# Kernel tuning notes

Hardware: AMD Instinct MI355X
Metric: run time of the kernel (lower is better)

## Reference

```python
import jax, jax.numpy as jnp
import numpy as np

B, S, D = 4, 2048, 512
H, DK, DV = 8, 64, 64
EPS = 1e-6
MASK_FILL = -1e-9  # faithful to the original masked_fill value (NOT -inf)


def setup_inputs() -> dict:
    key = jax.random.key(0)
    ks = jax.random.split(key, 9)
    sc = 0.05
    return {
        "q": jax.random.normal(ks[0], (B, S, D), jnp.float32),
        "k": jax.random.normal(ks[1], (B, S, D), jnp.float32),
        "v": jax.random.normal(ks[2], (B, S, D), jnp.float32),
        "src_mask": jax.random.randint(ks[3], (B, S), 0, 2, jnp.int32),
        "Wq": jax.random.normal(ks[4], (D, H * DK), jnp.float32) * sc,
        "Wk": jax.random.normal(ks[5], (D, H * DK), jnp.float32) * sc,
        "Wv": jax.random.normal(ks[6], (D, H * DV), jnp.float32) * sc,
        "Wo": jax.random.normal(ks[7], (H * DV, D), jnp.float32) * sc,
        "gamma": jnp.ones((D,), jnp.float32),
        "beta": jnp.zeros((D,), jnp.float32),
    }


def reference(q, k, v, src_mask, Wq, Wk, Wv, Wo, gamma, beta):
    b, len_q, _ = q.shape
    residual = q
    # QKV projections -> [B, H, S, dk/dv]
    qh = (q @ Wq).reshape(b, len_q, H, DK).transpose(0, 2, 1, 3)
    kh = (k @ Wk).reshape(b, -1, H, DK).transpose(0, 2, 1, 3)
    vh = (v @ Wv).reshape(b, -1, H, DV).transpose(0, 2, 1, 3)
    # scores [B, H, S, S]
    attn = jnp.einsum('bhqd,bhkd->bhqk', qh, kh) / jnp.sqrt(jnp.float32(DK))
    # pairwise src mask: outer product of [B,S] mask, diagonal forced to 1
    sm = src_mask[:, :len_q].astype(jnp.float32)
    am = sm[:, :, None] * sm[:, None, :]               # [B, S, S]
    idx = jnp.arange(len_q)
    am = am.at[:, idx, idx].set(1.0)
    attn = jnp.where(am[:, None, :, :] == 0, MASK_FILL, attn)
    attn = jax.nn.softmax(attn, axis=-1)
    out = jnp.einsum('bhqk,bhkd->bhqd', attn, vh)      # [B, H, S, dv]
    out = out.transpose(0, 2, 1, 3).reshape(b, len_q, H * DV)
    out = out @ Wo + residual
    # LayerNorm(eps=1e-6)
    mu = jnp.mean(out, axis=-1, keepdims=True)
    var = jnp.var(out, axis=-1, keepdims=True)
    out = (out - mu) * jax.lax.rsqrt(var + EPS) * gamma + beta
    return out, attn
```

## Files before the change

kernel.cpp:

```cpp
#include <hip/hip_runtime.h>
#include <math.h>

#define B_ 4
#define S_ 2048
#define D_ 512
#define H_ 8
#define NEG_FILL (-1e-9f)

typedef __attribute__((ext_vector_type(8))) short bf16x8;
typedef __attribute__((ext_vector_type(4))) float f32x4;

#define MFMA16(A, Bm, C) __builtin_amdgcn_mfma_f32_16x16x32_bf16((A), (Bm), (C), 0, 0, 0)

__device__ __forceinline__ short f2b(float f) {
  union { float f; unsigned u; } x;
  x.f = f;
  unsigned r = x.u + 0x7fffu + ((x.u >> 16) & 1u);
  return (short)(r >> 16);
}

__global__ __launch_bounds__(256) void prep_wt(
    const float* __restrict__ Wq, const float* __restrict__ Wk,
    const float* __restrict__ Wv, const float* __restrict__ Wo,
    short* __restrict__ Wqt, short* __restrict__ Wkt,
    short* __restrict__ Wvt, short* __restrict__ Wot)
{
  const float* W; short* Wt;
  switch (blockIdx.z) {
    case 0: W = Wq; Wt = Wqt; break;
    case 1: W = Wk; Wt = Wkt; break;
    case 2: W = Wv; Wt = Wvt; break;
    default: W = Wo; Wt = Wot; break;
  }
  __shared__ float Ws[64 * 68];
  const int t = threadIdx.x;
  const int n0 = blockIdx.x * 64, k0 = blockIdx.y * 64;

  #pragma unroll
  for (int rep = 0; rep < 4; ++rep) {
    int e4 = rep * 256 + t;
    int r = e4 >> 4, c0 = (e4 & 15) * 4;
    *(float4*)&Ws[r * 68 + c0] = *(const float4*)&W[(size_t)(k0 + r) * 512 + n0 + c0];
  }
  __syncthreads();

  int rn = t >> 2;
  int kb = (t & 3) * 16;
  union { short s[8]; int4 v; } pk;
  #pragma unroll
  for (int half = 0; half < 2; ++half) {
    #pragma unroll
    for (int i = 0; i < 8; ++i)
      pk.s[i] = f2b(Ws[(kb + half * 8 + i) * 68 + rn]);
    *(int4*)&Wt[(size_t)(n0 + rn) * 512 + k0 + kb + half * 8] = pk.v;
  }
}

__global__ __launch_bounds__(256) void qkv_mfma(
    const float* __restrict__ q, const float* __restrict__ k, const float* __restrict__ v,
    const short* __restrict__ Wqt, const short* __restrict__ Wkt, const short* __restrict__ Wvt,
    short* __restrict__ qh, short* __restrict__ kh, short* __restrict__ vt)
{
  const int z = blockIdx.z;
  const float* X = (z == 0) ? q : (z == 1) ? k : v;
  const short* Wt = (z == 0) ? Wqt : (z == 1) ? Wkt : Wvt;

  __shared__ short Xs[64 * 72];
  __shared__ short Wsh[64 * 72];

  const int t = threadIdx.x;
  const int wave = t >> 6, lane = t & 63, quad = lane >> 4, l15 = lane & 15;
  const int tile_n = blockIdx.x * 64;
  const int tile_m = blockIdx.y * 64;

  f32x4 acc[4];
  #pragma unroll
  for (int nt = 0; nt < 4; ++nt) acc[nt] = (f32x4){0.f, 0.f, 0.f, 0.f};

  for (int k0 = 0; k0 < 512; k0 += 64) {
    __syncthreads();
    #pragma unroll
    for (int rep = 0; rep < 4; ++rep) {
      int e4 = rep * 256 + t;
      int row = e4 >> 4, c0 = (e4 & 15) * 4;
      float4 xv = *(const float4*)&X[(size_t)(tile_m + row) * 512 + k0 + c0];
      *(short4*)&Xs[row * 72 + c0] =
          make_short4(f2b(xv.x), f2b(xv.y), f2b(xv.z), f2b(xv.w));
    }
    #pragma unroll
    for (int rep = 0; rep < 2; ++rep) {
      int e = rep * 256 + t;
      int row = e >> 3, c0 = (e & 7) * 8;
      *(int4*)&Wsh[row * 72 + c0] = *(const int4*)&Wt[(size_t)(tile_n + row) * 512 + k0 + c0];
    }
    __syncthreads();
    #pragma unroll
    for (int ks = 0; ks < 2; ++ks) {
      bf16x8 af = *(bf16x8*)&Xs[(wave * 16 + l15) * 72 + ks * 32 + quad * 8];
      #pragma unroll
      for (int nt = 0; nt < 4; ++nt) {
        bf16x8 bfr = *(bf16x8*)&Wsh[(nt * 16 + l15) * 72 + ks * 32 + quad * 8];
        acc[nt] = MFMA16(af, bfr, acc[nt]);
      }
    }
  }

  const int h = tile_n >> 6;
  if (z < 2) {
    short* Y = (z == 0) ? qh : kh;
    #pragma unroll
    for (int nt = 0; nt < 4; ++nt) {
      int d = nt * 16 + l15;
      #pragma unroll
      for (int r = 0; r < 4; ++r) {
        int row = tile_m + wave * 16 + quad * 4 + r;
        int b = row >> 11, s = row & (S_ - 1);
        Y[(((size_t)(b * H_ + h)) * S_ + s) * 64 + d] = f2b(acc[nt][r]);
      }
    }
  } else {
    int row0 = tile_m + wave * 16 + quad * 4;
    int b = row0 >> 11, s0 = row0 & (S_ - 1);
    #pragma unroll
    for (int nt = 0; nt < 4; ++nt) {
      int d = nt * 16 + l15;
      short4 pk = make_short4(f2b(acc[nt][0]), f2b(acc[nt][1]),
                              f2b(acc[nt][2]), f2b(acc[nt][3]));
      *(short4*)&vt[(((size_t)(b * H_ + h)) * 64 + d) * S_ + s0] = pk;
    }
  }
}

__global__ __launch_bounds__(256) void attn_mfma(
    const short* __restrict__ qh, const short* __restrict__ kh,
    const short* __restrict__ vt, const int* __restrict__ src_mask,
    float* __restrict__ attn_out, short* __restrict__ ohb)
{
  const int t = threadIdx.x;
  const int wave = t >> 6, lane = t & 63, quad = lane >> 4, l15 = lane & 15;

  const int lin = blockIdx.y * 32 + blockIdx.x;
  const int nl  = (lin & 7) * 128 + (lin >> 3);
  const int bh = nl >> 5, b = bh >> 3, h = bh & 7;
  const int q0 = (nl & 31) * 64;

  __shared__ __align__(16) short KV[4][64 * 64];
  __shared__ __align__(16) short Ps[4][16 * 72];
  __shared__ __align__(16) int smAll[S_];

  const short* __restrict__ khb = kh + (size_t)bh * S_ * 64;
  const short* __restrict__ vtb = vt + (size_t)bh * 64 * S_;

  const int sr = t >> 3, sc = t & 7;
  const int wofs0 = sr * 128 + ((sc ^ (sr & 7)) << 4);
  const int wofs1 = (sr + 32) * 128 + ((sc ^ (sr & 7)) << 4);
  const int rofs0 = ((quad ^ (l15 & 7)) << 4);
  const int rofs1 = (((4 + quad) ^ (l15 & 7)) << 4);

  const size_t qrow = (size_t)bh * S_ + q0 + wave * 16 + l15;
  const bf16x8 qf0 = *(const bf16x8*)&qh[qrow * 64 + quad * 8];
  const bf16x8 qf1 = *(const bf16x8*)&qh[qrow * 64 + 32 + quad * 8];

  int4 kreg0, kreg1, vreg0, vreg1;
  int4 mreg0 = *(const int4*)&src_mask[b * S_ + t * 4];
  int4 mreg1 = *(const int4*)&src_mask[b * S_ + (256 + t) * 4];
  kreg0 = *(const int4*)&khb[(size_t)sr * 64 + sc * 8];
  kreg1 = *(const int4*)&khb[(size_t)(sr + 32) * 64 + sc * 8];
  *(int4*)&smAll[t * 4] = mreg0;
  *(int4*)&smAll[(256 + t) * 4] = mreg1;
  *(int4*)((char*)KV[0] + wofs0) = kreg0;
  *(int4*)((char*)KV[0] + wofs1) = kreg1;
  __syncthreads();

  int rloc[4], mqr[4], qir[4];
  #pragma unroll
  for (int r = 0; r < 4; ++r) {
    rloc[r] = wave * 16 + quad * 4 + r;
    qir[r] = q0 + rloc[r];
    mqr[r] = smAll[qir[r]];
  }

  float rs[4] = {0.f, 0.f, 0.f, 0.f};
  for (int step = 0; step < 32; ++step) {
    const int kt0 = step * 64;
    const int cur = step & 1;
    if (step < 31) {
      kreg0 = *(const int4*)&khb[(size_t)(kt0 + 64 + sr) * 64 + sc * 8];
      kreg1 = *(const int4*)&khb[(size_t)(kt0 + 64 + sr + 32) * 64 + sc * 8];
    }
    const char* Kc = (const char*)KV[cur];
    #pragma unroll
    for (int nt = 0; nt < 4; ++nt) {
      bf16x8 kf0 = *(const bf16x8*)(Kc + (nt * 16 + l15) * 128 + rofs0);
      bf16x8 kf1 = *(const bf16x8*)(Kc + (nt * 16 + l15) * 128 + rofs1);
      f32x4 c = (f32x4){0.f, 0.f, 0.f, 0.f};
      c = MFMA16(qf0, kf0, c);
      c = MFMA16(qf1, kf1, c);
      int kj = kt0 + nt * 16 + l15;
      int mk = smAll[kj];
      #pragma unroll
      for (int r = 0; r < 4; ++r) {
        float ss = c[r] * 0.125f;
        bool keep = (mqr[r] & mk) || (qir[r] == kj);
        ss = keep ? ss : NEG_FILL;
        rs[r] += __expf(ss);
      }
    }
    if (step < 31) {
      *(int4*)((char*)KV[cur ^ 1] + wofs0) = kreg0;
      *(int4*)((char*)KV[cur ^ 1] + wofs1) = kreg1;
    }
    __syncthreads();
  }
  #pragma unroll
  for (int r = 0; r < 4; ++r) {
    float vsum = rs[r];
    vsum += __shfl_xor(vsum, 1);
    vsum += __shfl_xor(vsum, 2);
    vsum += __shfl_xor(vsum, 4);
    vsum += __shfl_xor(vsum, 8);
    rs[r] = 1.f / vsum;
  }

  f32x4 oacc[4];
  #pragma unroll
  for (int dt = 0; dt < 4; ++dt) oacc[dt] = (f32x4){0.f, 0.f, 0.f, 0.f};

  float* __restrict__ arow[4];
  #pragma unroll
  for (int r = 0; r < 4; ++r)
    arow[r] = attn_out + ((size_t)bh * S_ + q0 + rloc[r]) * S_;

  short* __restrict__ ps = Ps[wave];

  kreg0 = *(const int4*)&khb[(size_t)sr * 64 + sc * 8];
  kreg1 = *(const int4*)&khb[(size_t)(sr + 32) * 64 + sc * 8];
  vreg0 = *(const int4*)&vtb[(size_t)sr * S_ + sc * 8];
  vreg1 = *(const int4*)&vtb[(size_t)(sr + 32) * S_ + sc * 8];
  *(int4*)((char*)KV[0] + wofs0) = kreg0;
  *(int4*)((char*)KV[0] + wofs1) = kreg1;
  *(int4*)((char*)KV[2] + wofs0) = vreg0;
  *(int4*)((char*)KV[2] + wofs1) = vreg1;
  __syncthreads();

  for (int step = 0; step < 32; ++step) {
    const int kt0 = step * 64;
    const int cur = step & 1;
    if (step < 31) {
      kreg0 = *(const int4*)&khb[(size_t)(kt0 + 64 + sr) * 64 + sc * 8];
      kreg1 = *(const int4*)&khb[(size_t)(kt0 + 64 + sr + 32) * 64 + sc * 8];
      vreg0 = *(const int4*)&vtb[(size_t)sr * S_ + kt0 + 64 + sc * 8];
      vreg1 = *(const int4*)&vtb[(size_t)(sr + 32) * S_ + kt0 + 64 + sc * 8];
    }
    const char* Kc = (const char*)KV[cur];
    const char* Vc = (const char*)KV[2 + cur];
    #pragma unroll
    for (int nt = 0; nt < 4; ++nt) {
      bf16x8 kf0 = *(const bf16x8*)(Kc + (nt * 16 + l15) * 128 + rofs0);
      bf16x8 kf1 = *(const bf16x8*)(Kc + (nt * 16 + l15) * 128 + rofs1);
      f32x4 c = (f32x4){0.f, 0.f, 0.f, 0.f};
      c = MFMA16(qf0, kf0, c);
      c = MFMA16(qf1, kf1, c);
      int kj = kt0 + nt * 16 + l15;
      int mk = smAll[kj];
      #pragma unroll
      for (int r = 0; r < 4; ++r) {
        float ss = c[r] * 0.125f;
        bool keep = (mqr[r] & mk) || (qir[r] == kj);
        ss = keep ? ss : NEG_FILL;
        float p = __expf(ss) * rs[r];
        __builtin_nontemporal_store(p, &arow[r][kj]);
        ps[(quad * 4 + r) * 72 + nt * 16 + l15] = f2b(p);
      }
    }
    bf16x8 pf0 = *(bf16x8*)&ps[l15 * 72 + quad * 8];
    bf16x8 pf1 = *(bf16x8*)&ps[l15 * 72 + 32 + quad * 8];
    #pragma unroll
    for (int dt = 0; dt < 4; ++dt) {
      bf16x8 vf0 = *(const bf16x8*)(Vc + (dt * 16 + l15) * 128 + rofs0);
      bf16x8 vf1 = *(const bf16x8*)(Vc + (dt * 16 + l15) * 128 + rofs1);
      oacc[dt] = MFMA16(pf0, vf0, oacc[dt]);
      oacc[dt] = MFMA16(pf1, vf1, oacc[dt]);
    }
    if (step < 31) {
      *(int4*)((char*)KV[cur ^ 1] + wofs0) = kreg0;
      *(int4*)((char*)KV[cur ^ 1] + wofs1) = kreg1;
      *(int4*)((char*)KV[2 + (cur ^ 1)] + wofs0) = vreg0;
      *(int4*)((char*)KV[2 + (cur ^ 1)] + wofs1) = vreg1;
    }
    __syncthreads();
  }

  #pragma unroll
  for (int dt = 0; dt < 4; ++dt) {
    int d = h * 64 + dt * 16 + l15;
    #pragma unroll
    for (int r = 0; r < 4; ++r)
      ohb[((size_t)b * S_ + q0 + rloc[r]) * 512 + d] = f2b(oacc[dt][r]);
  }
}

__global__ __launch_bounds__(256) void out_mfma(
    const short* __restrict__ ohb, const short* __restrict__ Wot,
    const float* __restrict__ resid, float* __restrict__ out)
{
  __shared__ short Xs[64 * 72];
  __shared__ short Wsh[64 * 72];

  const int t = threadIdx.x;
  const int wave = t >> 6, lane = t & 63, quad = lane >> 4, l15 = lane & 15;
  const int tile_n = blockIdx.x * 64;
  const int tile_m = blockIdx.y * 64;

  f32x4 acc[4];
  #pragma unroll
  for (int nt = 0; nt < 4; ++nt) acc[nt] = (f32x4){0.f, 0.f, 0.f, 0.f};

  for (int k0 = 0; k0 < 512; k0 += 64) {
    __syncthreads();
    #pragma unroll
    for (int rep = 0; rep < 2; ++rep) {
      int e = rep * 256 + t;
      int row = e >> 3, c0 = (e & 7) * 8;
      *(int4*)&Xs[row * 72 + c0] = *(const int4*)&ohb[(size_t)(tile_m + row) * 512 + k0 + c0];
      *(int4*)&Wsh[row * 72 + c0] = *(const int4*)&Wot[(size_t)(tile_n + row) * 512 + k0 + c0];
    }
    __syncthreads();
    #pragma unroll
    for (int ks = 0; ks < 2; ++ks) {
      bf16x8 af = *(bf16x8*)&Xs[(wave * 16 + l15) * 72 + ks * 32 + quad * 8];
      #pragma unroll
      for (int nt = 0; nt < 4; ++nt) {
        bf16x8 bfr = *(bf16x8*)&Wsh[(nt * 16 + l15) * 72 + ks * 32 + quad * 8];
        acc[nt] = MFMA16(af, bfr, acc[nt]);
      }
    }
  }

  #pragma unroll
  for (int nt = 0; nt < 4; ++nt) {
    int c = tile_n + nt * 16 + l15;
    #pragma unroll
    for (int r = 0; r < 4; ++r) {
      size_t row = tile_m + wave * 16 + quad * 4 + r;
      out[row * 512 + c] = acc[nt][r] + resid[row * 512 + c];
    }
  }
}

__global__ __launch_bounds__(256) void ln_kernel(
    float* __restrict__ io, const float* __restrict__ gamma, const float* __restrict__ beta)
{
  const int wid  = threadIdx.x >> 6;
  const int lane = threadIdx.x & 63;
  const size_t row = (size_t)blockIdx.x * 4 + wid;
  const size_t base = row * 512 + lane * 8;

  float4 x0 = *(const float4*)&io[base];
  float4 x1 = *(const float4*)&io[base + 4];
  float xs[8] = {x0.x, x0.y, x0.z, x0.w, x1.x, x1.y, x1.z, x1.w};

  float s = 0.f, s2 = 0.f;
  #pragma unroll
  for (int i = 0; i < 8; ++i) { s += xs[i]; s2 = fmaf(xs[i], xs[i], s2); }
  #pragma unroll
  for (int m = 1; m < 64; m <<= 1) {
    s  += __shfl_xor(s, m);
    s2 += __shfl_xor(s2, m);
  }
  float mu  = s * (1.f / 512.f);
  float var = s2 * (1.f / 512.f) - mu * mu;
  float rsq = rsqrtf(var + 1e-6f);

  float4 g0 = *(const float4*)&gamma[lane * 8];
  float4 g1 = *(const float4*)&gamma[lane * 8 + 4];
  float4 b0 = *(const float4*)&beta[lane * 8];
  float4 b1 = *(const float4*)&beta[lane * 8 + 4];
  float gs[8] = {g0.x, g0.y, g0.z, g0.w, g1.x, g1.y, g1.z, g1.w};
  float bs[8] = {b0.x, b0.y, b0.z, b0.w, b1.x, b1.y, b1.z, b1.w};

  float ys[8];
  #pragma unroll
  for (int i = 0; i < 8; ++i) ys[i] = (xs[i] - mu) * rsq * gs[i] + bs[i];
  *(float4*)&io[base]     = make_float4(ys[0], ys[1], ys[2], ys[3]);
  *(float4*)&io[base + 4] = make_float4(ys[4], ys[5], ys[6], ys[7]);
}

extern "C" void kernel_launch(void* const* d_in, const int* in_sizes, int n_in,
                              void* d_out, int out_size, void* d_ws, size_t ws_size,
                              hipStream_t stream)
{
  const float* q     = (const float*)d_in[0];
  const float* k     = (const float*)d_in[1];
  const float* v     = (const float*)d_in[2];
  const int*  smask  = (const int*)d_in[3];
  const float* Wq    = (const float*)d_in[4];
  const float* Wk    = (const float*)d_in[5];
  const float* Wv    = (const float*)d_in[6];
  const float* Wo    = (const float*)d_in[7];
  const float* gamma = (const float*)d_in[8];
  const float* beta  = (const float*)d_in[9];

  float* out  = (float*)d_out;
  float* attn = out + (size_t)B_ * S_ * D_;

  short* wsS = (short*)d_ws;
  short* qh  = wsS;
  short* kh  = qh + 4194304;
  short* vt  = kh + 4194304;
  short* ohb = vt + 4194304;
  short* Wqt = ohb + 4194304;
  short* Wkt = Wqt + 262144;
  short* Wvt = Wkt + 262144;
  short* Wot = Wvt + 262144;

  prep_wt<<<dim3(8, 8, 4), 256, 0, stream>>>(Wq, Wk, Wv, Wo, Wqt, Wkt, Wvt, Wot);
  qkv_mfma<<<dim3(8, 128, 3), 256, 0, stream>>>(q, k, v, Wqt, Wkt, Wvt, qh, kh, vt);
  attn_mfma<<<dim3(32, 32), 256, 0, stream>>>(qh, kh, vt, smask, attn, ohb);
  out_mfma<<<dim3(8, 128), 256, 0, stream>>>(ohb, Wot, q, out);
  ln_kernel<<<2048, 256, 0, stream>>>(out, gamma, beta);
}
```

Measured before the change: 724.5 us.

## Enlarge QKV GEMM tiles to 128x128 and attention blocks to 128 queries

The QKV projection kernel moves from 64x64 to 128x128 output tiles, with each of its four waves computing a 64x64 sub-tile from a 4x4 set of MFMA accumulators, so each loaded X and W fragment is reused more. The attention kernel now runs 512 threads (8 waves) per block covering 128 query rows, so every K/V tile staged in shared memory serves twice as many queries and global K/V traffic per query is halved. In exchange, registers per thread rise in the GEMM, shared memory per block grows, and both kernels launch fewer blocks, which may lower occupancy.

```diff
diff --git a/kernel.cpp b/kernel.cpp
--- a/kernel.cpp
+++ b/kernel.cpp
@@ -65,22 +65,25 @@
   const float* X = (z == 0) ? q : (z == 1) ? k : v;
   const short* Wt = (z == 0) ? Wqt : (z == 1) ? Wkt : Wvt;
 
-  __shared__ short Xs[64 * 72];
-  __shared__ short Wsh[64 * 72];
+  __shared__ short Xs[128 * 72];
+  __shared__ short Wsh[128 * 72];
 
   const int t = threadIdx.x;
   const int wave = t >> 6, lane = t & 63, quad = lane >> 4, l15 = lane & 15;
-  const int tile_n = blockIdx.x * 64;
-  const int tile_m = blockIdx.y * 64;
-
-  f32x4 acc[4];
-  #pragma unroll
-  for (int nt = 0; nt < 4; ++nt) acc[nt] = (f32x4){0.f, 0.f, 0.f, 0.f};
+  const int wm = wave >> 1, wn = wave & 1;
+  const int tile_n = blockIdx.x * 128;
+  const int tile_m = blockIdx.y * 128;
+
+  f32x4 acc[4][4];
+  #pragma unroll
+  for (int mt = 0; mt < 4; ++mt)
+    #pragma unroll
+    for (int nt = 0; nt < 4; ++nt) acc[mt][nt] = (f32x4){0.f, 0.f, 0.f, 0.f};
 
   for (int k0 = 0; k0 < 512; k0 += 64) {
     __syncthreads();
     #pragma unroll
-    for (int rep = 0; rep < 4; ++rep) {
+    for (int rep = 0; rep < 8; ++rep) {
       int e4 = rep * 256 + t;
       int row = e4 >> 4, c0 = (e4 & 15) * 4;
       float4 xv = *(const float4*)&X[(size_t)(tile_m + row) * 512 + k0 + c0];
@@ -88,7 +91,7 @@
           make_short4(f2b(xv.x), f2b(xv.y), f2b(xv.z), f2b(xv.w));
     }
     #pragma unroll
-    for (int rep = 0; rep < 2; ++rep) {
+    for (int rep = 0; rep < 4; ++rep) {
       int e = rep * 256 + t;
       int row = e >> 3, c0 = (e & 7) * 8;
       *(int4*)&Wsh[row * 72 + c0] = *(const int4*)&Wt[(size_t)(tile_n + row) * 512 + k0 + c0];
@@ -96,42 +99,56 @@
     __syncthreads();
     #pragma unroll
     for (int ks = 0; ks < 2; ++ks) {
-      bf16x8 af = *(bf16x8*)&Xs[(wave * 16 + l15) * 72 + ks * 32 + quad * 8];
-      #pragma unroll
-      for (int nt = 0; nt < 4; ++nt) {
-        bf16x8 bfr = *(bf16x8*)&Wsh[(nt * 16 + l15) * 72 + ks * 32 + quad * 8];
-        acc[nt] = MFMA16(af, bfr, acc[nt]);
-      }
-    }
-  }
-
-  const int h = tile_n >> 6;
+      bf16x8 af[4], bfr[4];
+      #pragma unroll
+      for (int mt = 0; mt < 4; ++mt)
+        af[mt] = *(bf16x8*)&Xs[(wm * 64 + mt * 16 + l15) * 72 + ks * 32 + quad * 8];
+      #pragma unroll
+      for (int nt = 0; nt < 4; ++nt)
+        bfr[nt] = *(bf16x8*)&Wsh[(wn * 64 + nt * 16 + l15) * 72 + ks * 32 + quad * 8];
+      #pragma unroll
+      for (int mt = 0; mt < 4; ++mt)
+        #pragma unroll
+        for (int nt = 0; nt < 4; ++nt)
+          acc[mt][nt] = MFMA16(af[mt], bfr[nt], acc[mt][nt]);
+    }
+  }
+
+  const int col0 = tile_n + wn * 64;
   if (z < 2) {
     short* Y = (z == 0) ? qh : kh;
     #pragma unroll
     for (int nt = 0; nt < 4; ++nt) {
-      int d = nt * 16 + l15;
-      #pragma unroll
-      for (int r = 0; r < 4; ++r) {
-        int row = tile_m + wave * 16 + quad * 4 + r;
-        int b = row >> 11, s = row & (S_ - 1);
-        Y[(((size_t)(b * H_ + h)) * S_ + s) * 64 + d] = f2b(acc[nt][r]);
+      int cc = col0 + nt * 16 + l15;
+      int h = cc >> 6, d = cc & 63;
+      #pragma unroll
+      for (int mt = 0; mt < 4; ++mt) {
+        #pragma unroll
+        for (int r = 0; r < 4; ++r) {
+          int row = tile_m + wm * 64 + mt * 16 + quad * 4 + r;
+          int b = row >> 11, s = row & (S_ - 1);
+          Y[(((size_t)(b * H_ + h)) * S_ + s) * 64 + d] = f2b(acc[mt][nt][r]);
+        }
       }
     }
   } else {
-    int row0 = tile_m + wave * 16 + quad * 4;
-    int b = row0 >> 11, s0 = row0 & (S_ - 1);
     #pragma unroll
     for (int nt = 0; nt < 4; ++nt) {
-      int d = nt * 16 + l15;
-      short4 pk = make_short4(f2b(acc[nt][0]), f2b(acc[nt][1]),
-                              f2b(acc[nt][2]), f2b(acc[nt][3]));
-      *(short4*)&vt[(((size_t)(b * H_ + h)) * 64 + d) * S_ + s0] = pk;
-    }
-  }
-}
-
-__global__ __launch_bounds__(256) void attn_mfma(
+      int cc = col0 + nt * 16 + l15;
+      int h = cc >> 6, d = cc & 63;
+      #pragma unroll
+      for (int mt = 0; mt < 4; ++mt) {
+        int row0 = tile_m + wm * 64 + mt * 16 + quad * 4;
+        int b = row0 >> 11, s0 = row0 & (S_ - 1);
+        short4 pk = make_short4(f2b(acc[mt][nt][0]), f2b(acc[mt][nt][1]),
+                                f2b(acc[mt][nt][2]), f2b(acc[mt][nt][3]));
+        *(short4*)&vt[(((size_t)(b * H_ + h)) * 64 + d) * S_ + s0] = pk;
+      }
+    }
+  }
+}
+
+__global__ __launch_bounds__(512) void attn_mfma(
     const short* __restrict__ qh, const short* __restrict__ kh,
     const short* __restrict__ vt, const int* __restrict__ src_mask,
     float* __restrict__ attn_out, short* __restrict__ ohb)
@@ -139,21 +156,20 @@
   const int t = threadIdx.x;
   const int wave = t >> 6, lane = t & 63, quad = lane >> 4, l15 = lane & 15;
 
-  const int lin = blockIdx.y * 32 + blockIdx.x;
-  const int nl  = (lin & 7) * 128 + (lin >> 3);
-  const int bh = nl >> 5, b = bh >> 3, h = bh & 7;
-  const int q0 = (nl & 31) * 64;
+  const int lin = blockIdx.y * 16 + blockIdx.x;
+  const int nl  = (lin & 7) * 64 + (lin >> 3);
+  const int bh = nl >> 4, b = bh >> 3, h = bh & 7;
+  const int q0 = (nl & 15) * 128;
 
   __shared__ __align__(16) short KV[4][64 * 64];
-  __shared__ __align__(16) short Ps[4][16 * 72];
+  __shared__ __align__(16) short Ps[8][16 * 72];
   __shared__ __align__(16) int smAll[S_];
 
   const short* __restrict__ khb = kh + (size_t)bh * S_ * 64;
   const short* __restrict__ vtb = vt + (size_t)bh * 64 * S_;
 
   const int sr = t >> 3, sc = t & 7;
-  const int wofs0 = sr * 128 + ((sc ^ (sr & 7)) << 4);
-  const int wofs1 = (sr + 32) * 128 + ((sc ^ (sr & 7)) << 4);
+  const int wofs = sr * 128 + ((sc ^ (sr & 7)) << 4);
   const int rofs0 = ((quad ^ (l15 & 7)) << 4);
   const int rofs1 = (((4 + quad) ^ (l15 & 7)) << 4);
 
@@ -161,15 +177,11 @@
   const bf16x8 qf0 = *(const bf16x8*)&qh[qrow * 64 + quad * 8];
   const bf16x8 qf1 = *(const bf16x8*)&qh[qrow * 64 + 32 + quad * 8];
 
-  int4 kreg0, kreg1, vreg0, vreg1;
-  int4 mreg0 = *(const int4*)&src_mask[b * S_ + t * 4];
-  int4 mreg1 = *(const int4*)&src_mask[b * S_ + (256 + t) * 4];
-  kreg0 = *(const int4*)&khb[(size_t)sr * 64 + sc * 8];
-  kreg1 = *(const int4*)&khb[(size_t)(sr + 32) * 64 + sc * 8];
-  *(int4*)&smAll[t * 4] = mreg0;
-  *(int4*)&smAll[(256 + t) * 4] = mreg1;
-  *(int4*)((char*)KV[0] + wofs0) = kreg0;
-  *(int4*)((char*)KV[0] + wofs1) = kreg1;
+  int4 kreg, vreg;
+  int4 mreg = *(const int4*)&src_mask[b * S_ + t * 4];
+  kreg = *(const int4*)&khb[(size_t)sr * 64 + sc * 8];
+  *(int4*)&smAll[t * 4] = mreg;
+  *(int4*)((char*)KV[0] + wofs) = kreg;
   __syncthreads();
 
   int rloc[4], mqr[4], qir[4];
@@ -184,10 +196,8 @@
   for (int step = 0; step < 32; ++step) {
     const int kt0 = step * 64;
     const int cur = step & 1;
-    if (step < 31) {
-      kreg0 = *(const int4*)&khb[(size_t)(kt0 + 64 + sr) * 64 + sc * 8];
-      kreg1 = *(const int4*)&khb[(size_t)(kt0 + 64 + sr + 32) * 64 + sc * 8];
-    }
+    if (step < 31)
+      kreg = *(const int4*)&khb[(size_t)(kt0 + 64 + sr) * 64 + sc * 8];
     const char* Kc = (const char*)KV[cur];
     #pragma unroll
     for (int nt = 0; nt < 4; ++nt) {
@@ -206,10 +216,8 @@
         rs[r] += __expf(ss);
       }
     }
-    if (step < 31) {
-      *(int4*)((char*)KV[cur ^ 1] + wofs0) = kreg0;
-      *(int4*)((char*)KV[cur ^ 1] + wofs1) = kreg1;
-    }
+    if (step < 31)
+      *(int4*)((char*)KV[cur ^ 1] + wofs) = kreg;
     __syncthreads();
   }
   #pragma unroll
@@ -233,24 +241,18 @@
 
   short* __restrict__ ps = Ps[wave];
 
-  kreg0 = *(const int4*)&khb[(size_t)sr * 64 + sc * 8];
-  kreg1 = *(const int4*)&khb[(size_t)(sr + 32) * 64 + sc * 8];
-  vreg0 = *(const int4*)&vtb[(size_t)sr * S_ + sc * 8];
-  vreg1 = *(const int4*)&vtb[(size_t)(sr + 32) * S_ + sc * 8];
-  *(int4*)((char*)KV[0] + wofs0) = kreg0;
-  *(int4*)((char*)KV[0] + wofs1) = kreg1;
-  *(int4*)((char*)KV[2] + wofs0) = vreg0;
-  *(int4*)((char*)KV[2] + wofs1) = vreg1;
+  kreg = *(const int4*)&khb[(size_t)sr * 64 + sc * 8];
+  vreg = *(const int4*)&vtb[(size_t)sr * S_ + sc * 8];
+  *(int4*)((char*)KV[0] + wofs) = kreg;
+  *(int4*)((char*)KV[2] + wofs) = vreg;
   __syncthreads();
 
   for (int step = 0; step < 32; ++step) {
     const int kt0 = step * 64;
     const int cur = step & 1;
     if (step < 31) {
-      kreg0 = *(const int4*)&khb[(size_t)(kt0 + 64 + sr) * 64 + sc * 8];
-      kreg1 = *(const int4*)&khb[(size_t)(kt0 + 64 + sr + 32) * 64 + sc * 8];
-      vreg0 = *(const int4*)&vtb[(size_t)sr * S_ + kt0 + 64 + sc * 8];
-      vreg1 = *(const int4*)&vtb[(size_t)(sr + 32) * S_ + kt0 + 64 + sc * 8];
+      kreg = *(const int4*)&khb[(size_t)(kt0 + 64 + sr) * 64 + sc * 8];
+      vreg = *(const int4*)&vtb[(size_t)sr * S_ + kt0 + 64 + sc * 8];
     }
     const char* Kc = (const char*)KV[cur];
     const char* Vc = (const char*)KV[2 + cur];
@@ -283,10 +285,8 @@
       oacc[dt] = MFMA16(pf1, vf1, oacc[dt]);
     }
     if (step < 31) {
-      *(int4*)((char*)KV[cur ^ 1] + wofs0) = kreg0;
-      *(int4*)((char*)KV[cur ^ 1] + wofs1) = kreg1;
-      *(int4*)((char*)KV[2 + (cur ^ 1)] + wofs0) = vreg0;
-      *(int4*)((char*)KV[2 + (cur ^ 1)] + wofs1) = vreg1;
+      *(int4*)((char*)KV[cur ^ 1] + wofs) = kreg;
+      *(int4*)((char*)KV[2 + (cur ^ 1)] + wofs) = vreg;
     }
     __syncthreads();
   }
@@ -415,8 +415,8 @@
   short* Wot = Wvt + 262144;
 
   prep_wt<<<dim3(8, 8, 4), 256, 0, stream>>>(Wq, Wk, Wv, Wo, Wqt, Wkt, Wvt, Wot);
-  qkv_mfma<<<dim3(8, 128, 3), 256, 0, stream>>>(q, k, v, Wqt, Wkt, Wvt, qh, kh, vt);
-  attn_mfma<<<dim3(32, 32), 256, 0, stream>>>(qh, kh, vt, smask, attn, ohb);
+  qkv_mfma<<<dim3(4, 64, 3), 256, 0, stream>>>(q, k, v, Wqt, Wkt, Wvt, qh, kh, vt);
+  attn_mfma<<<dim3(16, 32), 512, 0, stream>>>(qh, kh, vt, smask, attn, ohb);
   out_mfma<<<dim3(8, 128), 256, 0, stream>>>(ohb, Wot, q, out);
   ln_kernel<<<2048, 256, 0, stream>>>(out, gamma, beta);
 }
```

New measurement: 745.0 us. +2.8%, slower.
